# Kernel optimization log

Hardware: AMD Instinct MI355X
Metric: run time of the kernel (lower is better)

## Reference

```python
import jax, jax.numpy as jnp
import numpy as np

H_SIZE = 1024
N_HEADS = 16
D_K = H_SIZE // N_HEADS


def setup_inputs() -> dict:
    key = jax.random.key(0)
    ks = jax.random.split(key, 12)
    s = 1.0 / np.sqrt(H_SIZE)
    inp = {
        "x": jax.random.normal(ks[0], (2, 2048, H_SIZE), dtype=jnp.float32),
        "Wq": jax.random.uniform(ks[1], (H_SIZE, H_SIZE), minval=-s, maxval=s),
        "bq": jax.random.uniform(ks[2], (H_SIZE,), minval=-s, maxval=s),
        "Wk": jax.random.uniform(ks[3], (H_SIZE, H_SIZE), minval=-s, maxval=s),
        "bk": jax.random.uniform(ks[4], (H_SIZE,), minval=-s, maxval=s),
        "Wv": jax.random.uniform(ks[5], (H_SIZE, H_SIZE), minval=-s, maxval=s),
        "bv": jax.random.uniform(ks[6], (H_SIZE,), minval=-s, maxval=s),
        "Wo": jax.random.uniform(ks[7], (H_SIZE, H_SIZE), minval=-s, maxval=s),
        "bo": jax.random.uniform(ks[8], (H_SIZE,), minval=-s, maxval=s),
        "ln_gamma": jnp.ones((H_SIZE,), dtype=jnp.float32),
        "ln_beta": jnp.zeros((H_SIZE,), dtype=jnp.float32),
    }
    return inp


def reference(x, Wq, bq, Wk, bk, Wv, bv, Wo, bo, ln_gamma, ln_beta):
    B, L, H = x.shape
    residual = x
    # QKV projections -> [B, n_heads, L, d_k]
    def proj(W, b):
        return (x @ W.T + b).reshape(B, L, N_HEADS, D_K).transpose(0, 2, 1, 3)
    q = proj(Wq, bq)
    k = proj(Wk, bk)
    v = proj(Wv, bv)
    # scaled dot-product attention (dropout = identity in eval mode)
    scores = jnp.einsum("bhqd,bhkd->bhqk", q, k) / jnp.sqrt(jnp.float32(D_K))
    attn = jax.nn.softmax(scores, axis=-1)
    out = jnp.einsum("bhqk,bhkd->bhqd", attn, v)
    out = out.transpose(0, 2, 1, 3).reshape(B, L, H)
    out = out @ Wo.T + bo
    # residual + LayerNorm
    y = out + residual
    mu = jnp.mean(y, axis=-1, keepdims=True)
    var = jnp.var(y, axis=-1, keepdims=True)
    y = (y - mu) / jnp.sqrt(var + 1e-5) * ln_gamma + ln_beta
    return y
```

## Files before the change

### kernel.cpp

```cpp
#include <hip/hip_runtime.h>

#define H_SIZE 1024
#define N_HEADS 16
#define D_K 64
#define SEQ 2048
#define BATCH 2
#define M_TOT 4096

typedef __bf16 __attribute__((ext_vector_type(8))) bf16_8;
typedef float __attribute__((ext_vector_type(4))) f32x4;
typedef float __attribute__((ext_vector_type(16))) f32x16;
typedef int __attribute__((ext_vector_type(4))) int4v;

#define SWZ(r) ((((r) & 7) ^ (((r) >> 3) & 7)))

__device__ __forceinline__ ushort f2bf(float f) {
    unsigned int u = __float_as_uint(f);
    unsigned int r = (u + 0x7FFFu + ((u >> 16) & 1u)) >> 16;
    return (ushort)r;
}

__device__ __forceinline__ unsigned int cvtpk(float lo, float hi) {
    unsigned int r;
    asm("v_cvt_pk_bf16_f32 %0, %1, %2" : "=v"(r) : "v"(lo), "v"(hi));
    return r;
}

__device__ __forceinline__ float exp2_raw(float x) {
    float r;
    asm("v_exp_f32 %0, %1" : "=v"(r) : "v"(x));
    return r;
}

__device__ __forceinline__ void gld16(void* lds, const void* g) {
    __builtin_amdgcn_global_load_lds(
        (const __attribute__((address_space(1))) unsigned int*)g,
        (__attribute__((address_space(3))) unsigned int*)lds, 16, 0, 0);
}

__global__ __launch_bounds__(256) void cast_all_kernel(
    const float* __restrict__ x, const float* __restrict__ wq, const float* __restrict__ wk,
    const float* __restrict__ wv, const float* __restrict__ wo,
    ushort* __restrict__ xb, ushort* __restrict__ wqb, ushort* __restrict__ wkb,
    ushort* __restrict__ wvb, ushort* __restrict__ wob) {
    int i = blockIdx.x * 256 + threadIdx.x;
    const float* src;
    ushort* dst;
    int off;
    if (i < 1048576) {
        src = x; dst = xb; off = i;
    } else {
        int j = i - 1048576;
        int w = j >> 18;
        off = j & 262143;
        src = (w == 0) ? wq : (w == 1) ? wk : (w == 2) ? wv : wo;
        dst = (w == 0) ? wqb : (w == 1) ? wkb : (w == 2) ? wvb : wob;
    }
    float4 v = ((const float4*)src)[off];
    ushort4 o;
    o.x = f2bf(v.x); o.y = f2bf(v.y); o.z = f2bf(v.z); o.w = f2bf(v.w);
    ((ushort4*)dst)[off] = o;
}

__global__ __launch_bounds__(256) void gemm_qkv(
    const ushort* __restrict__ A, const ushort* __restrict__ wq,
    const ushort* __restrict__ wk, const ushort* __restrict__ wv,
    const float* __restrict__ bq, const float* __restrict__ bk, const float* __restrict__ bv,
    ushort* __restrict__ Qb, ushort* __restrict__ Kb, ushort* __restrict__ Vtb) {
    __shared__ ushort As[2][128 * 64];
    __shared__ ushort Bs[2][128 * 64];
    const int tid = threadIdx.x;
    const int lane = tid & 63, wid = tid >> 6;
    const int wr = wid >> 1, wc = wid & 1;
    const int hi = lane >> 4, lo = lane & 15;
    const int bm0 = blockIdx.x * 128;
    const int t3 = blockIdx.y >> 3;
    const int bn0 = (blockIdx.y & 7) * 128;
    const ushort* Bw = (t3 == 0) ? wq : (t3 == 1) ? wk : wv;
    const float* bias = (t3 == 0) ? bq : (t3 == 1) ? bk : bv;

    f32x4 acc[4][4] = {};

    const int srow = tid >> 3;
    const int sseg = (tid & 7) * 8;
    const ushort* gaB = A + (size_t)(bm0 + srow) * H_SIZE + sseg;
    const ushort* gbB = Bw + (size_t)(bn0 + srow) * H_SIZE + sseg;
    const int ldsOff = tid * 16;

#define STAGE(bb, kt)                                                     \
    {                                                                     \
        char* la = (char*)&As[bb][0] + ldsOff;                            \
        char* lb = (char*)&Bs[bb][0] + ldsOff;                            \
        gld16(la, gaB + (kt));                                            \
        gld16(la + 4096, gaB + 32 * H_SIZE + (kt));                       \
        gld16(la + 8192, gaB + 64 * H_SIZE + (kt));                       \
        gld16(la + 12288, gaB + 96 * H_SIZE + (kt));                      \
        gld16(lb, gbB + (kt));                                            \
        gld16(lb + 4096, gbB + 32 * H_SIZE + (kt));                       \
        gld16(lb + 8192, gbB + 64 * H_SIZE + (kt));                       \
        gld16(lb + 12288, gbB + 96 * H_SIZE + (kt));                      \
    }

    STAGE(0, 0);
    __syncthreads();
    int cur = 0;
    constexpr int NT = H_SIZE / 64;
    for (int t = 0; t < NT; t++) {
        if (t + 1 < NT) STAGE(cur ^ 1, (t + 1) * 64);
#pragma unroll
        for (int kk = 0; kk < 64; kk += 32) {
            bf16_8 af[4], bfv[4];
            const ushort* pa = &As[cur][(wr * 64 + lo) * 64 + kk + hi * 8];
            const ushort* pb = &Bs[cur][(wc * 64 + lo) * 64 + kk + hi * 8];
#pragma unroll
            for (int i = 0; i < 4; i++) af[i] = *(const bf16_8*)(pa + i * 16 * 64);
#pragma unroll
            for (int i = 0; i < 4; i++) bfv[i] = *(const bf16_8*)(pb + i * 16 * 64);
#pragma unroll
            for (int mi = 0; mi < 4; mi++)
#pragma unroll
                for (int ni = 0; ni < 4; ni++)
                    acc[mi][ni] = __builtin_amdgcn_mfma_f32_16x16x32_bf16(
                        af[mi], bfv[ni], acc[mi][ni], 0, 0, 0);
        }
        __syncthreads();
        cur ^= 1;
    }
#undef STAGE

#pragma unroll
    for (int mi = 0; mi < 4; mi++) {
#pragma unroll
        for (int ni = 0; ni < 4; ni++) {
            const int row0 = bm0 + wr * 64 + mi * 16 + hi * 4;
            const int col = bn0 + wc * 64 + ni * 16 + lo;
            const float bv = bias[col];
            const int h = col >> 6, dk = col & 63;
            if (t3 == 2) {
                const int b = row0 >> 11, l0 = row0 & 2047;
                const int lsw0 = (l0 & ~63) | (((((l0 >> 3) & 7) ^ SWZ(dk)) & 7) << 3) | (l0 & 7);
                ushort4 o;
                o.x = f2bf(acc[mi][ni][0] + bv);
                o.y = f2bf(acc[mi][ni][1] + bv);
                o.z = f2bf(acc[mi][ni][2] + bv);
                o.w = f2bf(acc[mi][ni][3] + bv);
                *(ushort4*)&Vtb[((size_t)(b * N_HEADS + h) * D_K + dk) * SEQ + lsw0] = o;
            } else {
#pragma unroll
                for (int rr = 0; rr < 4; rr++) {
                    const int m = row0 + rr;
                    const int b = m >> 11, l = m & 2047;
                    float val = acc[mi][ni][rr] + bv;
                    if (t3 == 0) {
                        Qb[((size_t)(b * N_HEADS + h) * SEQ + l) * D_K + dk] =
                            f2bf(val * 0.18033688f);
                    } else {
                        int dks = ((((dk >> 3) ^ SWZ(l & 63)) & 7) << 3) | (dk & 7);
                        Kb[((size_t)(b * N_HEADS + h) * SEQ + l) * D_K + dks] = f2bf(val);
                    }
                }
            }
        }
    }
}

__global__ __launch_bounds__(256) void gemm_o(const ushort* __restrict__ A,
                                              const ushort* __restrict__ Bw,
                                              const float* __restrict__ bias,
                                              const float* __restrict__ resid,
                                              float* __restrict__ outp) {
    __shared__ ushort As[2][128 * 64];
    __shared__ ushort Bs[2][64 * 64];
    const int tid = threadIdx.x;
    const int lane = tid & 63, wid = tid >> 6;
    const int wr = wid >> 1, wc = wid & 1;
    const int hi = lane >> 4, lo = lane & 15;
    const int bm0 = blockIdx.x * 128, bn0 = blockIdx.y * 64;

    f32x4 acc[4][2] = {};

    const int srow = tid >> 3;
    const int sseg = (tid & 7) * 8;
    const ushort* gaB = A + (size_t)(bm0 + srow) * H_SIZE + sseg;
    const ushort* gbB = Bw + (size_t)(bn0 + srow) * H_SIZE + sseg;
    const int ldsOff = tid * 16;

#define STAGE(bb, kt)                                                     \
    {                                                                     \
        char* la = (char*)&As[bb][0] + ldsOff;                            \
        char* lb = (char*)&Bs[bb][0] + ldsOff;                            \
        gld16(la, gaB + (kt));                                            \
        gld16(la + 4096, gaB + 32 * H_SIZE + (kt));                       \
        gld16(la + 8192, gaB + 64 * H_SIZE + (kt));                       \
        gld16(la + 12288, gaB + 96 * H_SIZE + (kt));                      \
        gld16(lb, gbB + (kt));                                            \
        gld16(lb + 4096, gbB + 32 * H_SIZE + (kt));                       \
    }

    STAGE(0, 0);
    __syncthreads();
    int cur = 0;
    constexpr int NT = H_SIZE / 64;
    for (int t = 0; t < NT; t++) {
        if (t + 1 < NT) STAGE(cur ^ 1, (t + 1) * 64);
#pragma unroll
        for (int kk = 0; kk < 64; kk += 32) {
            bf16_8 af[4], bfv[2];
            const ushort* pa = &As[cur][(wr * 64 + lo) * 64 + kk + hi * 8];
            const ushort* pb = &Bs[cur][(wc * 32 + lo) * 64 + kk + hi * 8];
#pragma unroll
            for (int i = 0; i < 4; i++) af[i] = *(const bf16_8*)(pa + i * 16 * 64);
#pragma unroll
            for (int i = 0; i < 2; i++) bfv[i] = *(const bf16_8*)(pb + i * 16 * 64);
#pragma unroll
            for (int mi = 0; mi < 4; mi++)
#pragma unroll
                for (int ni = 0; ni < 2; ni++)
                    acc[mi][ni] = __builtin_amdgcn_mfma_f32_16x16x32_bf16(
                        af[mi], bfv[ni], acc[mi][ni], 0, 0, 0);
        }
        __syncthreads();
        cur ^= 1;
    }
#undef STAGE

#pragma unroll
    for (int mi = 0; mi < 4; mi++) {
#pragma unroll
        for (int ni = 0; ni < 2; ni++) {
            const int row0 = bm0 + wr * 64 + mi * 16 + hi * 4;
            const int col = bn0 + wc * 32 + ni * 16 + lo;
            const float bv = bias[col];
#pragma unroll
            for (int rr = 0; rr < 4; rr++) {
                const int m = row0 + rr;
                outp[(size_t)m * H_SIZE + col] =
                    acc[mi][ni][rr] + bv + resid[(size_t)m * H_SIZE + col];
            }
        }
    }
}

__global__ __launch_bounds__(256) void attn_kernel(const ushort* __restrict__ Q,
                                                   const ushort* __restrict__ Ksw,
                                                   const ushort* __restrict__ Vsw,
                                                   ushort* __restrict__ Out) {
    __shared__ ushort Ks[2][64 * 64];
    __shared__ ushort Vs[2][64 * 64];
    __shared__ float lsum_lds[4][32];
    const int lane = threadIdx.x & 63, wid = threadIdx.x >> 6;
    const int h32 = lane >> 5, q32 = lane & 31;
    const int bh = blockIdx.y;
    const int q0w = blockIdx.x * 128 + wid * 32;
    const ushort* Qh = Q + (size_t)bh * SEQ * D_K;
    const ushort* Kp = Ksw + (size_t)bh * SEQ * D_K;
    const ushort* Vp = Vsw + (size_t)bh * D_K * SEQ;

    bf16_8 qf[4];
#pragma unroll
    for (int tt = 0; tt < 4; tt++)
        qf[tt] = *(const bf16_8*)(Qh + (size_t)(q0w + q32) * D_K + tt * 16 + h32 * 8);

    f32x16 oacc0 = {}, oacc1 = {};
    float ls = 0.f;

    const int koff = wid * 2048 + lane * 16;
    const int vrow = wid * 16 + (lane >> 3);
    const int vseg = (lane & 7) * 16;

#define STAGE(bb, kt)                                                             \
    {                                                                             \
        const char* kg = (const char*)(Kp + (size_t)(kt) * D_K);                  \
        char* kl = (char*)&Ks[bb][0];                                             \
        gld16(kl + koff, kg + koff);                                              \
        gld16(kl + koff + 1024, kg + koff + 1024);                                \
        char* vl = (char*)&Vs[bb][0];                                             \
        gld16(vl + vrow * 128 + vseg,                                             \
              (const char*)(Vp + (size_t)vrow * SEQ + (kt)) + vseg);              \
        gld16(vl + (vrow + 8) * 128 + vseg,                                       \
              (const char*)(Vp + (size_t)(vrow + 8) * SEQ + (kt)) + vseg);        \
    }

    STAGE(0, 0);
    __syncthreads();
    int buf = 0;
    for (int t = 0; t < SEQ / 64; t++) {
        if (t + 1 < SEQ / 64) STAGE(buf ^ 1, (t + 1) * 64);
        const ushort* kb = &Ks[buf][0];
        const ushort* vb = &Vs[buf][0];
#pragma unroll
        for (int kh = 0; kh < 2; kh++) {
            f32x16 st = {};
            const int krow = kh * 32 + q32;
#pragma unroll
            for (int tt = 0; tt < 4; tt++) {
                int sg = (2 * tt + h32) ^ SWZ(krow);
                bf16_8 kf = *(const bf16_8*)(kb + krow * 64 + sg * 8);
                st = __builtin_amdgcn_mfma_f32_32x32x16_bf16(kf, qf[tt], st, 0, 0, 0);
            }
            float p[16];
#pragma unroll
            for (int rr = 0; rr < 16; rr++) p[rr] = exp2_raw(st[rr]);
            float partial = 0.f;
#pragma unroll
            for (int rr = 0; rr < 16; rr++) partial += p[rr];
            ls += partial + __shfl_xor(partial, 32);

            union { unsigned int w[4]; bf16_8 v; } pf0, pf1;
#pragma unroll
            for (int i = 0; i < 2; i++) {
                unsigned int a = cvtpk(p[2 * i], p[2 * i + 1]);
                unsigned int b = cvtpk(p[4 + 2 * i], p[4 + 2 * i + 1]);
                asm volatile("v_permlane32_swap_b32 %0, %1" : "+v"(a), "+v"(b));
                pf0.w[i] = a; pf0.w[2 + i] = b;
                unsigned int c = cvtpk(p[8 + 2 * i], p[8 + 2 * i + 1]);
                unsigned int d = cvtpk(p[12 + 2 * i], p[12 + 2 * i + 1]);
                asm volatile("v_permlane32_swap_b32 %0, %1" : "+v"(c), "+v"(d));
                pf1.w[i] = c; pf1.w[2 + i] = d;
            }

            {
                const int vr0 = q32;
                int sg0 = (4 * kh + h32) ^ SWZ(vr0);
                int sg1 = (4 * kh + 2 + h32) ^ SWZ(vr0);
                bf16_8 vf0 = *(const bf16_8*)(vb + vr0 * 64 + sg0 * 8);
                bf16_8 vf1 = *(const bf16_8*)(vb + vr0 * 64 + sg1 * 8);
                oacc0 = __builtin_amdgcn_mfma_f32_32x32x16_bf16(pf0.v, vf0, oacc0, 0, 0, 0);
                oacc0 = __builtin_amdgcn_mfma_f32_32x32x16_bf16(pf1.v, vf1, oacc0, 0, 0, 0);
            }
            {
                const int vr1 = 32 + q32;
                int sg0 = (4 * kh + h32) ^ SWZ(vr1);
                int sg1 = (4 * kh + 2 + h32) ^ SWZ(vr1);
                bf16_8 vf0 = *(const bf16_8*)(vb + vr1 * 64 + sg0 * 8);
                bf16_8 vf1 = *(const bf16_8*)(vb + vr1 * 64 + sg1 * 8);
                oacc1 = __builtin_amdgcn_mfma_f32_32x32x16_bf16(pf0.v, vf0, oacc1, 0, 0, 0);
                oacc1 = __builtin_amdgcn_mfma_f32_32x32x16_bf16(pf1.v, vf1, oacc1, 0, 0, 0);
            }
        }
        __syncthreads();
        buf ^= 1;
    }
#undef STAGE

    if (lane < 32) lsum_lds[wid][q32] = 1.0f / ls;
    const int b = bh >> 4, h = bh & 15;
#pragma unroll
    for (int rr = 0; rr < 16; rr++) {
        const int qloc = (rr & 3) + 8 * (rr >> 2) + 4 * h32;
        const float inv = lsum_lds[wid][qloc];
        const int l = q0w + qloc;
        ushort* orow = Out + ((size_t)(b * SEQ + l)) * H_SIZE + h * 64;
        orow[q32] = f2bf(oacc0[rr] * inv);
        orow[32 + q32] = f2bf(oacc1[rr] * inv);
    }
}

__global__ __launch_bounds__(256) void ln_kernel(float* __restrict__ y,
                                                 const float* __restrict__ gamma,
                                                 const float* __restrict__ beta) {
    const int row = blockIdx.x;
    float4* p = (float4*)(y + (size_t)row * H_SIZE);
    float4 v = p[threadIdx.x];
    float s = v.x + v.y + v.z + v.w;
    float s2 = v.x * v.x + v.y * v.y + v.z * v.z + v.w * v.w;
#pragma unroll
    for (int off = 1; off < 64; off <<= 1) {
        s += __shfl_xor(s, off);
        s2 += __shfl_xor(s2, off);
    }
    __shared__ float ss[4], ss2[4];
    const int wid = threadIdx.x >> 6, lane = threadIdx.x & 63;
    if (lane == 0) { ss[wid] = s; ss2[wid] = s2; }
    __syncthreads();
    s = ss[0] + ss[1] + ss[2] + ss[3];
    s2 = ss2[0] + ss2[1] + ss2[2] + ss2[3];
    const float mean = s * (1.0f / H_SIZE);
    const float var = s2 * (1.0f / H_SIZE) - mean * mean;
    const float rstd = rsqrtf(var + 1e-5f);
    const float4 g = ((const float4*)gamma)[threadIdx.x];
    const float4 bt = ((const float4*)beta)[threadIdx.x];
    float4 o;
    o.x = (v.x - mean) * rstd * g.x + bt.x;
    o.y = (v.y - mean) * rstd * g.y + bt.y;
    o.z = (v.z - mean) * rstd * g.z + bt.z;
    o.w = (v.w - mean) * rstd * g.w + bt.w;
    p[threadIdx.x] = o;
}

extern "C" void kernel_launch(void* const* d_in, const int* in_sizes, int n_in,
                              void* d_out, int out_size, void* d_ws, size_t ws_size,
                              hipStream_t stream) {
    const float* x = (const float*)d_in[0];
    const float* Wq = (const float*)d_in[1];
    const float* bq = (const float*)d_in[2];
    const float* Wk = (const float*)d_in[3];
    const float* bk = (const float*)d_in[4];
    const float* Wv = (const float*)d_in[5];
    const float* bv = (const float*)d_in[6];
    const float* Wo = (const float*)d_in[7];
    const float* bo = (const float*)d_in[8];
    const float* gamma = (const float*)d_in[9];
    const float* beta = (const float*)d_in[10];

    char* ws = (char*)d_ws;
    ushort* xb  = (ushort*)(ws);
    ushort* wqb = (ushort*)(ws + (8u << 20));
    ushort* wkb = (ushort*)(ws + (10u << 20));
    ushort* wvb = (ushort*)(ws + (12u << 20));
    ushort* wob = (ushort*)(ws + (14u << 20));
    ushort* Qb  = (ushort*)(ws + (16u << 20));
    ushort* Kb  = (ushort*)(ws + (24u << 20));
    ushort* Vtb = (ushort*)(ws + (32u << 20));
    ushort* Ao  = (ushort*)(ws + (40u << 20));

    cast_all_kernel<<<8192, 256, 0, stream>>>(x, Wq, Wk, Wv, Wo, xb, wqb, wkb, wvb, wob);

    dim3 gq(M_TOT / 128, 24);
    gemm_qkv<<<gq, 256, 0, stream>>>(xb, wqb, wkb, wvb, bq, bk, bv, Qb, Kb, Vtb);

    dim3 g2(SEQ / 128, BATCH * N_HEADS);
    attn_kernel<<<g2, 256, 0, stream>>>(Qb, Kb, Vtb, Ao);

    dim3 go(M_TOT / 128, H_SIZE / 64);
    gemm_o<<<go, 256, 0, stream>>>(Ao, wob, bo, x, (float*)d_out);

    ln_kernel<<<M_TOT, 256, 0, stream>>>((float*)d_out, gamma, beta);
}
```

Baseline: 155.4 us.

## Triple-buffer GEMM K-tiles with swizzled LDS and explicit vmcnt waits

Both projection GEMMs move from a double-buffered BK=64 loop to a triple-buffered BK=32 pipeline that prefetches two tiles ahead. Each iteration waits with explicit vmcnt counts plus raw barriers instead of __syncthreads draining all loads. An XOR swizzle on the LDS segment layout is meant to reduce bank conflicts on the fragment reads. The V store also switches to the packed bf16 convert instruction. The smaller K tile halves the MFMA work per barrier, so barrier overhead per unit of work grows.

Result: faster. 136.2 us (-12.4%).

```diff
diff --git a/kernel.cpp b/kernel.cpp
--- a/kernel.cpp
+++ b/kernel.cpp
@@ -67,8 +67,9 @@
     const ushort* __restrict__ wk, const ushort* __restrict__ wv,
     const float* __restrict__ bq, const float* __restrict__ bk, const float* __restrict__ bv,
     ushort* __restrict__ Qb, ushort* __restrict__ Kb, ushort* __restrict__ Vtb) {
-    __shared__ ushort As[2][128 * 64];
-    __shared__ ushort Bs[2][128 * 64];
+    constexpr int BK = 32;
+    __shared__ ushort As[3][128 * BK];
+    __shared__ ushort Bs[3][128 * BK];
     const int tid = threadIdx.x;
     const int lane = tid & 63, wid = tid >> 6;
     const int wr = wid >> 1, wc = wid & 1;
@@ -81,41 +82,42 @@
 
     f32x4 acc[4][4] = {};
 
-    const int srow = tid >> 3;
-    const int sseg = (tid & 7) * 8;
+    const int srow = tid >> 2;
+    const int sseg = ((tid & 3) ^ ((tid >> 3) & 3)) * 8;
     const ushort* gaB = A + (size_t)(bm0 + srow) * H_SIZE + sseg;
     const ushort* gbB = Bw + (size_t)(bn0 + srow) * H_SIZE + sseg;
     const int ldsOff = tid * 16;
 
-#define STAGE(bb, kt)                                                     \
-    {                                                                     \
-        char* la = (char*)&As[bb][0] + ldsOff;                            \
-        char* lb = (char*)&Bs[bb][0] + ldsOff;                            \
-        gld16(la, gaB + (kt));                                            \
-        gld16(la + 4096, gaB + 32 * H_SIZE + (kt));                       \
-        gld16(la + 8192, gaB + 64 * H_SIZE + (kt));                       \
-        gld16(la + 12288, gaB + 96 * H_SIZE + (kt));                      \
-        gld16(lb, gbB + (kt));                                            \
-        gld16(lb + 4096, gbB + 32 * H_SIZE + (kt));                       \
-        gld16(lb + 8192, gbB + 64 * H_SIZE + (kt));                       \
-        gld16(lb + 12288, gbB + 96 * H_SIZE + (kt));                      \
-    }
-
-    STAGE(0, 0);
-    __syncthreads();
+#define STAGE(ba, bb, kt)                                 \
+    {                                                     \
+        char* la = (char*)(ba) + ldsOff;                  \
+        char* lb = (char*)(bb) + ldsOff;                  \
+        gld16(la, gaB + (kt));                            \
+        gld16(la + 4096, gaB + 64 * H_SIZE + (kt));       \
+        gld16(lb, gbB + (kt));                            \
+        gld16(lb + 4096, gbB + 64 * H_SIZE + (kt));       \
+    }
+
+    STAGE(&As[0][0], &Bs[0][0], 0);
+    STAGE(&As[1][0], &Bs[1][0], BK);
+    asm volatile("s_waitcnt vmcnt(4)" ::: "memory");
+    __builtin_amdgcn_s_barrier();
+    __builtin_amdgcn_sched_barrier(0);
+
+    constexpr int NT = H_SIZE / BK;
+    const int rxv = (lo >> 1) & 3;
     int cur = 0;
-    constexpr int NT = H_SIZE / 64;
     for (int t = 0; t < NT; t++) {
-        if (t + 1 < NT) STAGE(cur ^ 1, (t + 1) * 64);
-#pragma unroll
-        for (int kk = 0; kk < 64; kk += 32) {
+        int c2 = cur + 2; if (c2 >= 3) c2 -= 3;
+        if (t + 2 < NT) STAGE(&As[c2][0], &Bs[c2][0], (t + 2) * BK);
+        {
             bf16_8 af[4], bfv[4];
-            const ushort* pa = &As[cur][(wr * 64 + lo) * 64 + kk + hi * 8];
-            const ushort* pb = &Bs[cur][(wc * 64 + lo) * 64 + kk + hi * 8];
-#pragma unroll
-            for (int i = 0; i < 4; i++) af[i] = *(const bf16_8*)(pa + i * 16 * 64);
-#pragma unroll
-            for (int i = 0; i < 4; i++) bfv[i] = *(const bf16_8*)(pb + i * 16 * 64);
+            const ushort* pa = &As[cur][(wr * 64 + lo) * BK + ((hi ^ rxv) * 8)];
+            const ushort* pb = &Bs[cur][(wc * 64 + lo) * BK + ((hi ^ rxv) * 8)];
+#pragma unroll
+            for (int i = 0; i < 4; i++) af[i] = *(const bf16_8*)(pa + i * 16 * BK);
+#pragma unroll
+            for (int i = 0; i < 4; i++) bfv[i] = *(const bf16_8*)(pb + i * 16 * BK);
 #pragma unroll
             for (int mi = 0; mi < 4; mi++)
 #pragma unroll
@@ -123,8 +125,13 @@
                     acc[mi][ni] = __builtin_amdgcn_mfma_f32_16x16x32_bf16(
                         af[mi], bfv[ni], acc[mi][ni], 0, 0, 0);
         }
-        __syncthreads();
-        cur ^= 1;
+        if (t + 1 < NT) {
+            if (t + 2 < NT) { asm volatile("s_waitcnt vmcnt(4)" ::: "memory"); }
+            else            { asm volatile("s_waitcnt vmcnt(0)" ::: "memory"); }
+            __builtin_amdgcn_s_barrier();
+            __builtin_amdgcn_sched_barrier(0);
+        }
+        cur = cur + 1; if (cur >= 3) cur -= 3;
     }
 #undef STAGE
 
@@ -139,12 +146,10 @@
             if (t3 == 2) {
                 const int b = row0 >> 11, l0 = row0 & 2047;
                 const int lsw0 = (l0 & ~63) | (((((l0 >> 3) & 7) ^ SWZ(dk)) & 7) << 3) | (l0 & 7);
-                ushort4 o;
-                o.x = f2bf(acc[mi][ni][0] + bv);
-                o.y = f2bf(acc[mi][ni][1] + bv);
-                o.z = f2bf(acc[mi][ni][2] + bv);
-                o.w = f2bf(acc[mi][ni][3] + bv);
-                *(ushort4*)&Vtb[((size_t)(b * N_HEADS + h) * D_K + dk) * SEQ + lsw0] = o;
+                uint2 o;
+                o.x = cvtpk(acc[mi][ni][0] + bv, acc[mi][ni][1] + bv);
+                o.y = cvtpk(acc[mi][ni][2] + bv, acc[mi][ni][3] + bv);
+                *(uint2*)&Vtb[((size_t)(b * N_HEADS + h) * D_K + dk) * SEQ + lsw0] = o;
             } else {
 #pragma unroll
                 for (int rr = 0; rr < 4; rr++) {
@@ -169,8 +174,9 @@
                                               const float* __restrict__ bias,
                                               const float* __restrict__ resid,
                                               float* __restrict__ outp) {
-    __shared__ ushort As[2][128 * 64];
-    __shared__ ushort Bs[2][64 * 64];
+    constexpr int BK = 32;
+    __shared__ ushort As[3][128 * BK];
+    __shared__ ushort Bs[3][64 * BK];
     const int tid = threadIdx.x;
     const int lane = tid & 63, wid = tid >> 6;
     const int wr = wid >> 1, wc = wid & 1;
@@ -179,39 +185,40 @@
 
     f32x4 acc[4][2] = {};
 
-    const int srow = tid >> 3;
-    const int sseg = (tid & 7) * 8;
+    const int srow = tid >> 2;
+    const int sseg = ((tid & 3) ^ ((tid >> 3) & 3)) * 8;
     const ushort* gaB = A + (size_t)(bm0 + srow) * H_SIZE + sseg;
     const ushort* gbB = Bw + (size_t)(bn0 + srow) * H_SIZE + sseg;
     const int ldsOff = tid * 16;
 
-#define STAGE(bb, kt)                                                     \
-    {                                                                     \
-        char* la = (char*)&As[bb][0] + ldsOff;                            \
-        char* lb = (char*)&Bs[bb][0] + ldsOff;                            \
-        gld16(la, gaB + (kt));                                            \
-        gld16(la + 4096, gaB + 32 * H_SIZE + (kt));                       \
-        gld16(la + 8192, gaB + 64 * H_SIZE + (kt));                       \
-        gld16(la + 12288, gaB + 96 * H_SIZE + (kt));                      \
-        gld16(lb, gbB + (kt));                                            \
-        gld16(lb + 4096, gbB + 32 * H_SIZE + (kt));                       \
-    }
-
-    STAGE(0, 0);
-    __syncthreads();
+#define STAGE(ba, bb, kt)                                 \
+    {                                                     \
+        char* la = (char*)(ba) + ldsOff;                  \
+        gld16(la, gaB + (kt));                            \
+        gld16(la + 4096, gaB + 64 * H_SIZE + (kt));       \
+        gld16((char*)(bb) + ldsOff, gbB + (kt));          \
+    }
+
+    STAGE(&As[0][0], &Bs[0][0], 0);
+    STAGE(&As[1][0], &Bs[1][0], BK);
+    asm volatile("s_waitcnt vmcnt(3)" ::: "memory");
+    __builtin_amdgcn_s_barrier();
+    __builtin_amdgcn_sched_barrier(0);
+
+    constexpr int NT = H_SIZE / BK;
+    const int rxv = (lo >> 1) & 3;
     int cur = 0;
-    constexpr int NT = H_SIZE / 64;
     for (int t = 0; t < NT; t++) {
-        if (t + 1 < NT) STAGE(cur ^ 1, (t + 1) * 64);
-#pragma unroll
-        for (int kk = 0; kk < 64; kk += 32) {
+        int c2 = cur + 2; if (c2 >= 3) c2 -= 3;
+        if (t + 2 < NT) STAGE(&As[c2][0], &Bs[c2][0], (t + 2) * BK);
+        {
             bf16_8 af[4], bfv[2];
-            const ushort* pa = &As[cur][(wr * 64 + lo) * 64 + kk + hi * 8];
-            const ushort* pb = &Bs[cur][(wc * 32 + lo) * 64 + kk + hi * 8];
-#pragma unroll
-            for (int i = 0; i < 4; i++) af[i] = *(const bf16_8*)(pa + i * 16 * 64);
-#pragma unroll
-            for (int i = 0; i < 2; i++) bfv[i] = *(const bf16_8*)(pb + i * 16 * 64);
+            const ushort* pa = &As[cur][(wr * 64 + lo) * BK + ((hi ^ rxv) * 8)];
+            const ushort* pb = &Bs[cur][(wc * 32 + lo) * BK + ((hi ^ rxv) * 8)];
+#pragma unroll
+            for (int i = 0; i < 4; i++) af[i] = *(const bf16_8*)(pa + i * 16 * BK);
+#pragma unroll
+            for (int i = 0; i < 2; i++) bfv[i] = *(const bf16_8*)(pb + i * 16 * BK);
 #pragma unroll
             for (int mi = 0; mi < 4; mi++)
 #pragma unroll
@@ -219,8 +226,13 @@
                     acc[mi][ni] = __builtin_amdgcn_mfma_f32_16x16x32_bf16(
                         af[mi], bfv[ni], acc[mi][ni], 0, 0, 0);
         }
-        __syncthreads();
-        cur ^= 1;
+        if (t + 1 < NT) {
+            if (t + 2 < NT) { asm volatile("s_waitcnt vmcnt(3)" ::: "memory"); }
+            else            { asm volatile("s_waitcnt vmcnt(0)" ::: "memory"); }
+            __builtin_amdgcn_s_barrier();
+            __builtin_amdgcn_sched_barrier(0);
+        }
+        cur = cur + 1; if (cur >= 3) cur -= 3;
     }
 #undef STAGE
 
```
